# Kernel optimization log

Measured on AMD Instinct MI355X. Metric: run time of the kernel, lower is better.

The kernel has to match this reference:

```python
import jax, jax.numpy as jnp
import numpy as np

MAX_ITER = 10
TAU = 1.0

def setup_inputs() -> dict:
    key = jax.random.key(0)
    s = jax.random.normal(key, (8192, 8192), dtype=jnp.float32)
    return {"s": s}

def reference(s) -> jnp.ndarray:
    # pygmtools sinkhorn (log-space): scale by 1/tau, then alternate
    # row-normalization (even iters) and column-normalization (odd iters)
    # via log-softmax; finally exponentiate.
    log_s = s / TAU
    for it in range(MAX_ITER):
        axis = 1 if it % 2 == 0 else 0  # rows first, then columns
        log_s = jax.nn.log_softmax(log_s, axis=axis)
    return jnp.exp(log_s)
```

## Files before the change

kernel.cpp:

```cpp
#include <hip/hip_runtime.h>
#include <math.h>

#define N 8192
#define NF4 2048


__device__ __forceinline__ float wave_max(float m) {
#pragma unroll
  for (int off = 32; off > 0; off >>= 1) m = fmaxf(m, __shfl_xor(m, off, 64));
  return m;
}
__device__ __forceinline__ float wave_sum(float s) {
#pragma unroll
  for (int off = 32; off > 0; off >>= 1) s += __shfl_xor(s, off, 64);
  return s;
}

template <int R>
__global__ __launch_bounds__(512, 8) void fused_pass(
    const float* __restrict__ s, const float* __restrict__ v,
    float* __restrict__ u, float* __restrict__ pt, int use_v) {
  const int t = threadIdx.x;
  const int wid = t >> 6, lane = t & 63;
  const int row0 = blockIdx.x * R;
  __shared__ float4 vsh[NF4];
  __shared__ float red[16];

  if (use_v) {
    const float4* v4 = (const float4*)v;
#pragma unroll
    for (int k = 0; k < 4; ++k) vsh[t + k * 512] = v4[t + k * 512];
  } else {
    const float4 z = make_float4(0.f, 0.f, 0.f, 0.f);
#pragma unroll
    for (int k = 0; k < 4; ++k) vsh[t + k * 512] = z;
  }

  float4 acc[4];
#pragma unroll
  for (int k = 0; k < 4; ++k) acc[k] = make_float4(0.f, 0.f, 0.f, 0.f);

  const float4* s4 = (const float4*)s + (size_t)row0 * NF4 + t;

#pragma unroll 1
  for (int r = 0; r < R; ++r) {
    float4 b[4];
#pragma unroll
    for (int k = 0; k < 4; ++k) b[k] = s4[(size_t)r * NF4 + k * 512];
    float m0 = -INFINITY, m1 = -INFINITY, m2 = -INFINITY, m3 = -INFINITY;
#pragma unroll
    for (int k = 0; k < 4; ++k) {
      const float4 vv = vsh[t + k * 512];
      b[k].x -= vv.x; b[k].y -= vv.y; b[k].z -= vv.z; b[k].w -= vv.w;
      m0 = fmaxf(m0, b[k].x); m1 = fmaxf(m1, b[k].y);
      m2 = fmaxf(m2, b[k].z); m3 = fmaxf(m3, b[k].w);
    }
    const float m = wave_max(fmaxf(fmaxf(m0, m1), fmaxf(m2, m3)));
    if (lane == 0) red[wid] = m;
    __syncthreads();
    float bm = red[0];
#pragma unroll
    for (int w = 1; w < 8; ++w) bm = fmaxf(bm, red[w]);
    float s0 = 0.f, s1 = 0.f, s2 = 0.f, s3 = 0.f;
#pragma unroll
    for (int k = 0; k < 4; ++k) {
      b[k].x = __expf(b[k].x - bm); b[k].y = __expf(b[k].y - bm);
      b[k].z = __expf(b[k].z - bm); b[k].w = __expf(b[k].w - bm);
      s0 += b[k].x; s1 += b[k].y; s2 += b[k].z; s3 += b[k].w;
    }
    const float ss = wave_sum((s0 + s1) + (s2 + s3));
    if (lane == 0) red[8 + wid] = ss;
    __syncthreads();
    float tot = red[8];
#pragma unroll
    for (int w = 1; w < 8; ++w) tot += red[8 + w];
    if (t == 0) u[row0 + r] = bm + __logf(tot);
    const float inv = 1.0f / tot;
#pragma unroll
    for (int k = 0; k < 4; ++k) {
      acc[k].x = fmaf(b[k].x, inv, acc[k].x);
      acc[k].y = fmaf(b[k].y, inv, acc[k].y);
      acc[k].z = fmaf(b[k].z, inv, acc[k].z);
      acc[k].w = fmaf(b[k].w, inv, acc[k].w);
    }
  }

  float4* p4 = (float4*)(pt + (size_t)blockIdx.x * N);
#pragma unroll
  for (int k = 0; k < 4; ++k) p4[t + k * 512] = acc[k];
}

__global__ __launch_bounds__(256) void combine1(const float* __restrict__ pt,
                                                float* __restrict__ ps,
                                                int per_group) {
  const int j = blockIdx.x * 256 + threadIdx.x;
  const int g = blockIdx.y;
  const float* p = pt + (size_t)g * per_group * N + j;
  float acc = 0.f;
  for (int c = 0; c < per_group; ++c) acc += p[(size_t)c * N];
  ps[(size_t)g * N + j] = acc;
}

__global__ __launch_bounds__(256) void combine2(const float* __restrict__ ps,
                                                float* __restrict__ v,
                                                int ngroups, int add_old) {
  const int j = blockIdx.x * 256 + threadIdx.x;
  float T = 0.f;
  for (int g = 0; g < ngroups; ++g) T += ps[(size_t)g * N + j];
  const float lv = __logf(T);
  v[j] = add_old ? v[j] + lv : lv;
}

__global__ __launch_bounds__(256) void finalize_k(const float* __restrict__ s,
                                                  const float* __restrict__ u,
                                                  const float* __restrict__ v,
                                                  float* __restrict__ out) {
  const size_t idx = (size_t)blockIdx.x * 256 + threadIdx.x;
  const int row = (int)(idx >> 11);
  const int c4 = (int)(idx & 2047);
  const float4 sv = ((const float4*)s)[idx];
  const float4 vv = ((const float4*)v)[c4];
  const float ur = u[row];
  float4 o;
  o.x = __expf(sv.x - ur - vv.x);
  o.y = __expf(sv.y - ur - vv.y);
  o.z = __expf(sv.z - ur - vv.z);
  o.w = __expf(sv.w - ur - vv.w);
  ((float4*)out)[idx] = o;
}

extern "C" void kernel_launch(void* const* d_in, const int* in_sizes, int n_in,
                              void* d_out, int out_size, void* d_ws, size_t ws_size,
                              hipStream_t stream) {
  const float* s = (const float*)d_in[0];
  float* out = (float*)d_out;
  float* ws = (float*)d_ws;

  const size_t avail = ws_size / sizeof(float);
  int nstrips = 512;
  while (nstrips > 128 && (size_t)(10 + nstrips) * N > avail) nstrips >>= 1;
  float* u = ws;
  float* v = ws + N;
  float* ps = ws + 2 * N;
  float* pt = ws + 10 * N;
  const int G = 8;
  const int per_group = nstrips / G;

  for (int p = 0; p < 5; ++p) {
    const int use_v = p > 0 ? 1 : 0;
    switch (nstrips) {
      case 512:
        fused_pass<16><<<512, 512, 0, stream>>>(s, v, u, pt, use_v);
        break;
      case 256:
        fused_pass<32><<<256, 512, 0, stream>>>(s, v, u, pt, use_v);
        break;
      default:
        fused_pass<64><<<128, 512, 0, stream>>>(s, v, u, pt, use_v);
        break;
    }
    combine1<<<dim3(N / 256, G), 256, 0, stream>>>(pt, ps, per_group);
    combine2<<<N / 256, 256, 0, stream>>>(ps, v, G, p > 0 ? 1 : 0);
  }
  finalize_k<<<(N / 256) * NF4, 256, 0, stream>>>(s, u, v, out);
}
```

Before: 799.5 us.

## Replace per-row max reduction with previous u shift and pipeline row loads

The row pass no longer computes a block-wide max. It uses the previous pass's row log-normaliser u as the stabilising shift, which removes one barrier and one wave reduction per row. Rows are double-buffered in registers so the next row's load overlaps processing of the current one, and v lives in registers instead of LDS. The two-stage column combine is merged into one kernel that reads all strips. The risk is overflow or underflow in exp if the stale shift drifts far from the true row max, plus higher register pressure from the launch-bounds change and full unrolling.

```diff
diff --git a/kernel.cpp b/kernel.cpp
--- a/kernel.cpp
+++ b/kernel.cpp
@@ -5,11 +5,6 @@
 #define NF4 2048
 
 
-__device__ __forceinline__ float wave_max(float m) {
-#pragma unroll
-  for (int off = 32; off > 0; off >>= 1) m = fmaxf(m, __shfl_xor(m, off, 64));
-  return m;
-}
 __device__ __forceinline__ float wave_sum(float s) {
 #pragma unroll
   for (int off = 32; off > 0; off >>= 1) s += __shfl_xor(s, off, 64);
@@ -17,64 +12,63 @@
 }
 
 template <int R>
-__global__ __launch_bounds__(512, 8) void fused_pass(
+__global__ __launch_bounds__(512, 4) void fused_pass(
     const float* __restrict__ s, const float* __restrict__ v,
-    float* __restrict__ u, float* __restrict__ pt, int use_v) {
+    float* __restrict__ u, float* __restrict__ pt, int pass0) {
   const int t = threadIdx.x;
   const int wid = t >> 6, lane = t & 63;
   const int row0 = blockIdx.x * R;
-  __shared__ float4 vsh[NF4];
-  __shared__ float red[16];
+  __shared__ float red[2][8];
 
-  if (use_v) {
+  float4 vv[4];
+  if (pass0) {
+#pragma unroll
+    for (int k = 0; k < 4; ++k) vv[k] = make_float4(0.f, 0.f, 0.f, 0.f);
+  } else {
     const float4* v4 = (const float4*)v;
 #pragma unroll
-    for (int k = 0; k < 4; ++k) vsh[t + k * 512] = v4[t + k * 512];
-  } else {
-    const float4 z = make_float4(0.f, 0.f, 0.f, 0.f);
+    for (int k = 0; k < 4; ++k) vv[k] = v4[t + k * 512];
+  }
+
+  float csh[R];
 #pragma unroll
-    for (int k = 0; k < 4; ++k) vsh[t + k * 512] = z;
-  }
+  for (int i = 0; i < R; ++i) csh[i] = pass0 ? 0.f : u[row0 + i];
 
   float4 acc[4];
 #pragma unroll
   for (int k = 0; k < 4; ++k) acc[k] = make_float4(0.f, 0.f, 0.f, 0.f);
 
   const float4* s4 = (const float4*)s + (size_t)row0 * NF4 + t;
+  float4 A[4], B[4];
 
-#pragma unroll 1
-  for (int r = 0; r < R; ++r) {
-    float4 b[4];
+  auto LOADA = [&](int r) {
 #pragma unroll
-    for (int k = 0; k < 4; ++k) b[k] = s4[(size_t)r * NF4 + k * 512];
-    float m0 = -INFINITY, m1 = -INFINITY, m2 = -INFINITY, m3 = -INFINITY;
+    for (int k = 0; k < 4; ++k) A[k] = s4[(size_t)r * NF4 + k * 512];
+  };
+  auto LOADB = [&](int r) {
 #pragma unroll
-    for (int k = 0; k < 4; ++k) {
-      const float4 vv = vsh[t + k * 512];
-      b[k].x -= vv.x; b[k].y -= vv.y; b[k].z -= vv.z; b[k].w -= vv.w;
-      m0 = fmaxf(m0, b[k].x); m1 = fmaxf(m1, b[k].y);
-      m2 = fmaxf(m2, b[k].z); m3 = fmaxf(m3, b[k].w);
-    }
-    const float m = wave_max(fmaxf(fmaxf(m0, m1), fmaxf(m2, m3)));
-    if (lane == 0) red[wid] = m;
-    __syncthreads();
-    float bm = red[0];
-#pragma unroll
-    for (int w = 1; w < 8; ++w) bm = fmaxf(bm, red[w]);
+    for (int k = 0; k < 4; ++k) B[k] = s4[(size_t)r * NF4 + k * 512];
+  };
+  auto PROC = [&](float4(&b)[4], int r) {
+    const float c = csh[r];
     float s0 = 0.f, s1 = 0.f, s2 = 0.f, s3 = 0.f;
 #pragma unroll
     for (int k = 0; k < 4; ++k) {
-      b[k].x = __expf(b[k].x - bm); b[k].y = __expf(b[k].y - bm);
-      b[k].z = __expf(b[k].z - bm); b[k].w = __expf(b[k].w - bm);
+      b[k].x = __expf(b[k].x - vv[k].x - c);
+      b[k].y = __expf(b[k].y - vv[k].y - c);
+      b[k].z = __expf(b[k].z - vv[k].z - c);
+      b[k].w = __expf(b[k].w - vv[k].w - c);
       s0 += b[k].x; s1 += b[k].y; s2 += b[k].z; s3 += b[k].w;
     }
     const float ss = wave_sum((s0 + s1) + (s2 + s3));
-    if (lane == 0) red[8 + wid] = ss;
-    __syncthreads();
-    float tot = red[8];
+    if (lane == 0) red[r & 1][wid] = ss;
+    asm volatile("s_waitcnt lgkmcnt(0)" ::: "memory");
+    __builtin_amdgcn_s_barrier();
+    asm volatile("" ::: "memory");
+    float tot = red[r & 1][0];
 #pragma unroll
-    for (int w = 1; w < 8; ++w) tot += red[8 + w];
-    if (t == 0) u[row0 + r] = bm + __logf(tot);
+    for (int w = 1; w < 8; ++w) tot += red[r & 1][w];
+    if (t == 0) u[row0 + r] = c + __logf(tot);
     const float inv = 1.0f / tot;
 #pragma unroll
     for (int k = 0; k < 4; ++k) {
@@ -83,6 +77,15 @@
       acc[k].z = fmaf(b[k].z, inv, acc[k].z);
       acc[k].w = fmaf(b[k].w, inv, acc[k].w);
     }
+  };
+
+  LOADA(0);
+#pragma unroll
+  for (int r = 0; r < R; r += 2) {
+    LOADB(r + 1);
+    PROC(A, r);
+    if (r + 2 < R) LOADA(r + 2);
+    PROC(B, r + 1);
   }
 
   float4* p4 = (float4*)(pt + (size_t)blockIdx.x * N);
@@ -90,23 +93,20 @@
   for (int k = 0; k < 4; ++k) p4[t + k * 512] = acc[k];
 }
 
-__global__ __launch_bounds__(256) void combine1(const float* __restrict__ pt,
-                                                float* __restrict__ ps,
-                                                int per_group) {
+__global__ __launch_bounds__(256) void combine(const float* __restrict__ pt,
+                                               float* __restrict__ v,
+                                               int nstrips, int add_old) {
   const int j = blockIdx.x * 256 + threadIdx.x;
-  const int g = blockIdx.y;
-  const float* p = pt + (size_t)g * per_group * N + j;
-  float acc = 0.f;
-  for (int c = 0; c < per_group; ++c) acc += p[(size_t)c * N];
-  ps[(size_t)g * N + j] = acc;
-}
-
-__global__ __launch_bounds__(256) void combine2(const float* __restrict__ ps,
-                                                float* __restrict__ v,
-                                                int ngroups, int add_old) {
-  const int j = blockIdx.x * 256 + threadIdx.x;
-  float T = 0.f;
-  for (int g = 0; g < ngroups; ++g) T += ps[(size_t)g * N + j];
+  float T0 = 0.f, T1 = 0.f, T2 = 0.f, T3 = 0.f;
+  int c = 0;
+  for (; c + 4 <= nstrips; c += 4) {
+    T0 += pt[(size_t)(c + 0) * N + j];
+    T1 += pt[(size_t)(c + 1) * N + j];
+    T2 += pt[(size_t)(c + 2) * N + j];
+    T3 += pt[(size_t)(c + 3) * N + j];
+  }
+  float T = (T0 + T1) + (T2 + T3);
+  for (; c < nstrips; ++c) T += pt[(size_t)c * N + j];
   const float lv = __logf(T);
   v[j] = add_old ? v[j] + lv : lv;
 }
@@ -138,29 +138,25 @@
 
   const size_t avail = ws_size / sizeof(float);
   int nstrips = 512;
-  while (nstrips > 128 && (size_t)(10 + nstrips) * N > avail) nstrips >>= 1;
+  while (nstrips > 128 && (size_t)(2 + nstrips) * N > avail) nstrips >>= 1;
   float* u = ws;
   float* v = ws + N;
-  float* ps = ws + 2 * N;
-  float* pt = ws + 10 * N;
-  const int G = 8;
-  const int per_group = nstrips / G;
+  float* pt = ws + 2 * N;
 
   for (int p = 0; p < 5; ++p) {
-    const int use_v = p > 0 ? 1 : 0;
+    const int pass0 = (p == 0) ? 1 : 0;
     switch (nstrips) {
       case 512:
-        fused_pass<16><<<512, 512, 0, stream>>>(s, v, u, pt, use_v);
+        fused_pass<16><<<512, 512, 0, stream>>>(s, v, u, pt, pass0);
         break;
       case 256:
-        fused_pass<32><<<256, 512, 0, stream>>>(s, v, u, pt, use_v);
+        fused_pass<32><<<256, 512, 0, stream>>>(s, v, u, pt, pass0);
         break;
       default:
-        fused_pass<64><<<128, 512, 0, stream>>>(s, v, u, pt, use_v);
+        fused_pass<64><<<128, 512, 0, stream>>>(s, v, u, pt, pass0);
         break;
     }
-    combine1<<<dim3(N / 256, G), 256, 0, stream>>>(pt, ps, per_group);
-    combine2<<<N / 256, 256, 0, stream>>>(ps, v, G, p > 0 ? 1 : 0);
+    combine<<<N / 256, 256, 0, stream>>>(pt, v, nstrips, p > 0 ? 1 : 0);
   }
   finalize_k<<<(N / 256) * NF4, 256, 0, stream>>>(s, u, v, out);
 }
```

Result: slower. 1.279 ms (+60.0%).
